# Kernel optimization log

Hardware: AMD Instinct MI355X
Metric: run time of the kernel (lower is better)

Reference implementation:

```python
import jax, jax.numpy as jnp
import numpy as np


def setup_inputs() -> dict:
    key = jax.random.key(0)
    kq, kk, kv = jax.random.split(key, 3)
    B, L, H, D = 2, 4096, 8, 64
    queries = jax.random.normal(kq, (B, L, H, D), dtype=jnp.float32)
    keys = jax.random.normal(kk, (B, L, H, D), dtype=jnp.float32)
    values = jax.random.normal(kv, (B, L, H, D), dtype=jnp.float32)
    return {"queries": queries, "keys": keys, "values": values}


def reference(queries, keys, values):
    # queries/keys/values: [B, L, H, D]
    d_model = queries.shape[-1]
    scale = 1.0 / jnp.sqrt(jnp.asarray(d_model, dtype=queries.dtype))
    # scores: [B, H, Lq, Lk]
    scores = jnp.einsum('blhd,bshd->bhls', queries, keys)
    # dropout is identity in eval mode / for deterministic reference
    A = jax.nn.softmax(scale * scores, axis=-1)
    # output: [B, Lq, H, D]
    V = jnp.einsum('bhls,bshd->blhd', A, values)
    return V
```

## Files before the change

### kernel.cpp

```cpp
#include <hip/hip_runtime.h>

#define Bn 2
#define Ln 4096
#define Hn 8
#define Dn 64
#define NMEGA 32
#define BH_STRIDE 262144

typedef float    f32x4  __attribute__((ext_vector_type(4)));
typedef float    f32x16 __attribute__((ext_vector_type(16)));
typedef _Float16 f16x2  __attribute__((ext_vector_type(2)));
typedef _Float16 f16x8  __attribute__((ext_vector_type(8)));
typedef unsigned int u32;
typedef u32 u32x2 __attribute__((ext_vector_type(2)));
typedef u32 u32x4 __attribute__((ext_vector_type(4)));

static __device__ __forceinline__ void gld16(const void* g, void* l){
    __builtin_amdgcn_global_load_lds(
        (const __attribute__((address_space(1))) unsigned int*)g,
        (__attribute__((address_space(3))) unsigned int*)l, 16, 0, 0);
}

static __device__ __forceinline__ u32 pkf16(float a, float b){
    auto h = __builtin_amdgcn_cvt_pkrtz(a, b);
    return __builtin_bit_cast(u32, h);
}

static __device__ __forceinline__ u32x2 swp(u32 a, u32 b){
    auto r = __builtin_amdgcn_permlane32_swap(a, b, false, false);
    return __builtin_bit_cast(u32x2, r);
}

__global__ __launch_bounds__(256)
void kvprep(const float* __restrict__ Kg, const float* __restrict__ Vg,
            _Float16* __restrict__ kp, _Float16* __restrict__ vp){
    const int t2 = blockIdx.x, bh = blockIdx.y, b = bh>>3, h = bh&7;
    const int tid = threadIdx.x;
    const int w = tid >> 6, lane = tid & 63;
    const int l31 = lane & 31, hi = lane >> 5;
    const int t = t2 >> 1, g = t2 & 1;

    {
        const float* ks = Kg + (((size_t)b*Ln + t2*32 + l31)*Hn + h)*Dn + w*16 + hi*8;
        float4 a  = *(const float4*)ks;
        float4 c4 = *(const float4*)(ks + 4);
        f16x8 o;
        o[0]=(_Float16)a.x;  o[1]=(_Float16)a.y;  o[2]=(_Float16)a.z;  o[3]=(_Float16)a.w;
        o[4]=(_Float16)c4.x; o[5]=(_Float16)c4.y; o[6]=(_Float16)c4.z; o[7]=(_Float16)c4.w;
        *(f16x8*)(kp + (size_t)bh*BH_STRIDE + (size_t)t*4096
                     + (size_t)(g*4 + w)*512 + (size_t)lane*8) = o;
    }

    {
        const int kh = w >> 1, dt = w & 1;
        const float* vs = Vg + (((size_t)b*Ln + t2*32 + kh*16 + hi*8)*Hn + h)*Dn
                        + dt*32 + l31;
        f16x8 o;
#pragma unroll
        for(int j=0;j<8;++j) o[j] = (_Float16)vs[(size_t)j*Hn*Dn];
        *(f16x8*)(vp + (size_t)bh*BH_STRIDE + (size_t)t*4096
                     + (size_t)(g*4 + w)*512 + (size_t)lane*8) = o;
    }
}

static __device__ __forceinline__ f32x16 qk4(const f16x8 (&kf)[4], const f16x8 (&qf)[4]){
    f32x16 s;
#pragma unroll
    for(int r=0;r<16;++r) s[r]=0.f;
    s = __builtin_amdgcn_mfma_f32_32x32x16_f16(kf[0], qf[0], s, 0,0,0);
    s = __builtin_amdgcn_mfma_f32_32x32x16_f16(kf[1], qf[1], s, 0,0,0);
    s = __builtin_amdgcn_mfma_f32_32x32x16_f16(kf[2], qf[2], s, 0,0,0);
    s = __builtin_amdgcn_mfma_f32_32x32x16_f16(kf[3], qf[3], s, 0,0,0);
    return s;
}

static __device__ __forceinline__ void finish_pv(const f32x16& S, float& lac,
                                                 f32x16& o0, f32x16& o1,
                                                 const f16x8 (&vf)[4]){
    f32x16 p;
#pragma unroll
    for(int r=0;r<16;++r) p[r] = __builtin_amdgcn_exp2f(S[r]);
    u32 A0 = pkf16(p[0],p[1]),   A1 = pkf16(p[2],p[3]);
    u32 B0 = pkf16(p[4],p[5]),   B1 = pkf16(p[6],p[7]);
    u32 C0 = pkf16(p[8],p[9]),   C1 = pkf16(p[10],p[11]);
    u32 D0 = pkf16(p[12],p[13]), D1 = pkf16(p[14],p[15]);
    u32x2 r0 = swp(A0,B0), r1 = swp(A1,B1);
    u32x2 r2 = swp(C0,D0), r3 = swp(C1,D1);
    u32x4 w0 = {r0.x, r1.x, r0.y, r1.y};
    u32x4 w1 = {r2.x, r3.x, r2.y, r3.y};
    f16x8 pa0 = __builtin_bit_cast(f16x8, w0);
    f16x8 pa1 = __builtin_bit_cast(f16x8, w1);
    const f16x2 ones = {(_Float16)1.0f, (_Float16)1.0f};
#pragma unroll
    for(int j=0;j<4;++j){
        f16x2 c0 = {pa0[2*j], pa0[2*j+1]};
        f16x2 c1 = {pa1[2*j], pa1[2*j+1]};
        lac = __builtin_amdgcn_fdot2(c0, ones, lac, false);
        lac = __builtin_amdgcn_fdot2(c1, ones, lac, false);
    }
    o0 = __builtin_amdgcn_mfma_f32_32x32x16_f16(pa0, vf[0], o0, 0,0,0);
    o0 = __builtin_amdgcn_mfma_f32_32x32x16_f16(pa1, vf[2], o0, 0,0,0);
    o1 = __builtin_amdgcn_mfma_f32_32x32x16_f16(pa0, vf[1], o1, 0,0,0);
    o1 = __builtin_amdgcn_mfma_f32_32x32x16_f16(pa1, vf[3], o1, 0,0,0);
}

__global__ __launch_bounds__(256,2)
void attn_fwd(const float* __restrict__ Qg, float* __restrict__ Og,
              const _Float16* __restrict__ kp, const _Float16* __restrict__ vp){
    __shared__ __align__(16) float xo[8448];
    _Float16* sKV = (_Float16*)xo;

    const int tid  = threadIdx.x;
    const int lane = tid & 63, wv = tid >> 6;
    const int kh2 = wv >> 1, g = wv & 1;
    const int l31 = lane & 31, hi = lane >> 5;
    const int bh = blockIdx.x, b = bh>>3, h = bh&7;
    const int q0 = blockIdx.y*64;

    const float c = 0.125f * 1.4426950408889634f;

    f16x8 qf[2][4];
#pragma unroll
    for(int qt=0;qt<2;++qt){
        const float* qrow = Qg + (((size_t)b*Ln + q0 + qt*32 + l31)*Hn + h)*Dn;
#pragma unroll
        for(int cc=0;cc<4;++cc){
            const float* p4 = qrow + cc*16 + hi*8;
            float4 x = *(const float4*)p4;
            float4 y = *(const float4*)(p4+4);
            f16x8 f;
            f[0]=(_Float16)(x.x*c); f[1]=(_Float16)(x.y*c);
            f[2]=(_Float16)(x.z*c); f[3]=(_Float16)(x.w*c);
            f[4]=(_Float16)(y.x*c); f[5]=(_Float16)(y.y*c);
            f[6]=(_Float16)(y.z*c); f[7]=(_Float16)(y.w*c);
            qf[qt][cc]=f;
        }
    }

    f32x16 o[2][2];
    float lac[2] = {0.f, 0.f};
#pragma unroll
    for(int qt=0;qt<2;++qt)
#pragma unroll
        for(int dt=0;dt<2;++dt)
#pragma unroll
            for(int r=0;r<16;++r) o[qt][dt][r]=0.f;

    const _Float16* kg = kp + (size_t)bh*BH_STRIDE;
    const _Float16* vg = vp + (size_t)bh*BH_STRIDE;

    const char* sKb = (const char*)sKV + kh2*8192 + g*4096 + lane*16;
    const char* sVb = sKb + 16384;

#pragma unroll
    for(int i=0;i<4;++i){
        int u = i*256 + tid;
        gld16(kg + (size_t)u*8, sKV + (size_t)u*8);
        gld16(vg + (size_t)u*8, sKV + 8192 + (size_t)u*8);
    }

    for(int T=0; T<NMEGA; ++T){
        __syncthreads();
        f16x8 kf[4], vf[4];
#pragma unroll
        for(int i=0;i<4;++i){
            kf[i] = *(const f16x8*)(sKb + (i<<10));
            vf[i] = *(const f16x8*)(sVb + (i<<10));
        }
        __syncthreads();
        if(T+1 < NMEGA){
            const _Float16* kgn = kg + (size_t)(T+1)*8192;
            const _Float16* vgn = vg + (size_t)(T+1)*8192;
#pragma unroll
            for(int i=0;i<4;++i){
                int u = i*256 + tid;
                gld16(kgn + (size_t)u*8, sKV + (size_t)u*8);
                gld16(vgn + (size_t)u*8, sKV + 8192 + (size_t)u*8);
            }
        }
        f32x16 S0 = qk4(kf, qf[0]);
        f32x16 S1 = qk4(kf, qf[1]);
        finish_pv(S0, lac[0], o[0][0], o[0][1], vf);
        finish_pv(S1, lac[1], o[1][0], o[1][1], vf);
    }

    float lred[2];
#pragma unroll
    for(int qt=0;qt<2;++qt)
        lred[qt] = lac[qt] + __shfl_xor(lac[qt], 32, 64);

    __syncthreads();
    float* xb0 = xo;
    float* xb1 = xo + 4096;
    float* xl0 = xo + 8192;
    float* xl1 = xo + 8256;

    if(g==1){
        float* xb = kh2 ? xb1 : xb0;
        float* xl = kh2 ? xl1 : xl0;
#pragma unroll
        for(int qt=0;qt<2;++qt){
#pragma unroll
            for(int dt=0;dt<2;++dt)
#pragma unroll
                for(int r=0;r<16;++r){
                    int qr = (r&3) + 8*(r>>2) + 4*hi;
                    xb[(qt*32 + qr)*64 + dt*32 + l31] = o[qt][dt][r];
                }
            if(hi==0) xl[qt*32 + l31] = lred[qt];
        }
    }
    __syncthreads();
    if(g==0){
        float* xb = kh2 ? xb1 : xb0;
        float* xl = kh2 ? xl1 : xl0;
#pragma unroll
        for(int qt=0;qt<2;++qt){
#pragma unroll
            for(int dt=0;dt<2;++dt)
#pragma unroll
                for(int r=0;r<16;++r){
                    int qr = (r&3) + 8*(r>>2) + 4*hi;
                    o[qt][dt][r] += xb[(qt*32 + qr)*64 + dt*32 + l31];
                }
            lred[qt] += xl[qt*32 + l31];
        }
    }
    __syncthreads();
    if(wv==2){
#pragma unroll
        for(int qt=0;qt<2;++qt){
#pragma unroll
            for(int dt=0;dt<2;++dt)
#pragma unroll
                for(int r=0;r<16;++r){
                    int qr = (r&3) + 8*(r>>2) + 4*hi;
                    xb0[(qt*32 + qr)*64 + dt*32 + l31] = o[qt][dt][r];
                }
            if(hi==0) xl0[qt*32 + l31] = lred[qt];
        }
    }
    __syncthreads();
    if(wv==0){
#pragma unroll
        for(int qt=0;qt<2;++qt){
            float inv = 1.0f/(lred[qt] + xl0[qt*32 + l31]);
            float* ob = Og + (((size_t)b*Ln + q0 + qt*32)*Hn + h)*Dn;
#pragma unroll
            for(int r=0;r<16;++r){
                int qr = (r&3) + 8*(r>>2) + 4*hi;
                float invr = __shfl(inv, qr, 64);
                float v0 = o[qt][0][r] + xb0[(qt*32 + qr)*64 +  0 + l31];
                float v1 = o[qt][1][r] + xb0[(qt*32 + qr)*64 + 32 + l31];
                ob[(size_t)qr*Hn*Dn +  0 + l31] = v0*invr;
                ob[(size_t)qr*Hn*Dn + 32 + l31] = v1*invr;
            }
        }
    }
}

extern "C" void kernel_launch(void* const* d_in, const int* in_sizes, int n_in,
                              void* d_out, int out_size, void* d_ws, size_t ws_size,
                              hipStream_t stream) {
    const float* Q = (const float*)d_in[0];
    const float* K = (const float*)d_in[1];
    const float* V = (const float*)d_in[2];
    float* O = (float*)d_out;

    _Float16* kp = (_Float16*)d_ws;
    _Float16* vp = (_Float16*)((char*)d_ws + (8u<<20));

    kvprep<<<dim3(128, 16), dim3(256), 0, stream>>>(K, V, kp, vp);
    attn_fwd<<<dim3(16, 64), dim3(256), 0, stream>>>(Q, O, kp, vp);
}
```

Baseline: 178.1 us.

## Give each wave a private LDS staging slice and drop block barriers in main loop

Each wave now loads only the K/V fragments it consumes into its own LDS region, so the two __syncthreads per iteration are replaced by per-wave s_waitcnt vmcnt/lgkmcnt waits. This removes block-wide barrier stalls and lets waves drift independently. The global_load_lds path's asynchronous LDS write is assumed complete after vmcnt(0), which relies on hardware ordering semantics. The cooperative coalesced load pattern is lost in favour of per-wave contiguous chunks.

```diff
diff --git a/kernel.cpp b/kernel.cpp
--- a/kernel.cpp
+++ b/kernel.cpp
@@ -108,14 +108,16 @@
 void attn_fwd(const float* __restrict__ Qg, float* __restrict__ Og,
               const _Float16* __restrict__ kp, const _Float16* __restrict__ vp){
     __shared__ __align__(16) float xo[8448];
-    _Float16* sKV = (_Float16*)xo;
-
     const int tid  = threadIdx.x;
     const int lane = tid & 63, wv = tid >> 6;
     const int kh2 = wv >> 1, g = wv & 1;
     const int l31 = lane & 31, hi = lane >> 5;
     const int bh = blockIdx.x, b = bh>>3, h = bh&7;
     const int q0 = blockIdx.y*64;
+
+    _Float16* sW = (_Float16*)xo + (size_t)wv*4096;
+    _Float16* sK = sW + (size_t)lane*8;
+    _Float16* sV = sW + 2048 + (size_t)lane*8;
 
     const float c = 0.125f * 1.4426950408889634f;
 
@@ -146,36 +148,31 @@
 #pragma unroll
             for(int r=0;r<16;++r) o[qt][dt][r]=0.f;
 
-    const _Float16* kg = kp + (size_t)bh*BH_STRIDE;
-    const _Float16* vg = vp + (size_t)bh*BH_STRIDE;
-
-    const char* sKb = (const char*)sKV + kh2*8192 + g*4096 + lane*16;
-    const char* sVb = sKb + 16384;
+    const _Float16* kq = kp + (size_t)bh*BH_STRIDE + kh2*4096 + g*2048 + (size_t)lane*8;
+    const _Float16* vq = vp + (size_t)bh*BH_STRIDE + kh2*4096 + g*2048 + (size_t)lane*8;
 
 #pragma unroll
     for(int i=0;i<4;++i){
-        int u = i*256 + tid;
-        gld16(kg + (size_t)u*8, sKV + (size_t)u*8);
-        gld16(vg + (size_t)u*8, sKV + 8192 + (size_t)u*8);
+        gld16(kq + i*512, sK + i*512);
+        gld16(vq + i*512, sV + i*512);
     }
 
     for(int T=0; T<NMEGA; ++T){
-        __syncthreads();
+        asm volatile("s_waitcnt vmcnt(0)" ::: "memory");
         f16x8 kf[4], vf[4];
 #pragma unroll
         for(int i=0;i<4;++i){
-            kf[i] = *(const f16x8*)(sKb + (i<<10));
-            vf[i] = *(const f16x8*)(sVb + (i<<10));
-        }
-        __syncthreads();
+            kf[i] = *(const f16x8*)(sK + i*512);
+            vf[i] = *(const f16x8*)(sV + i*512);
+        }
+        asm volatile("s_waitcnt lgkmcnt(0)" ::: "memory");
         if(T+1 < NMEGA){
-            const _Float16* kgn = kg + (size_t)(T+1)*8192;
-            const _Float16* vgn = vg + (size_t)(T+1)*8192;
+            const _Float16* kn = kq + (size_t)(T+1)*8192;
+            const _Float16* vn = vq + (size_t)(T+1)*8192;
 #pragma unroll
             for(int i=0;i<4;++i){
-                int u = i*256 + tid;
-                gld16(kgn + (size_t)u*8, sKV + (size_t)u*8);
-                gld16(vgn + (size_t)u*8, sKV + 8192 + (size_t)u*8);
+                gld16(kn + i*512, sK + i*512);
+                gld16(vn + i*512, sV + i*512);
             }
         }
         f32x16 S0 = qk4(kf, qf[0]);
```

Measured after the change: 172.4 us. 1.03x faster.
